# Performance work log

Measured on AMD Instinct MI355X. Metric: run time of the kernel, lower is better.

Reference implementation:

```python
import jax, jax.numpy as jnp
import numpy as np

N_NODES = 50000

# DGL ChebConv with k=2 and the standard lambda_max=2 approximation:
#   L_hat = L - I = -D^{-1/2} A D^{-1/2}
#   X0 = X ; X1 = L_hat @ X ; out = concat([X0, X1], -1) @ W + b
# Norm uses in-degrees (DGL behavior).

def setup_inputs() -> dict:
    key = jax.random.key(0)
    ks = jax.random.split(key, 8)
    E = 800000
    src = jax.random.randint(ks[0], (E,), 0, N_NODES, dtype=jnp.int32)
    dst = jax.random.randint(ks[1], (E,), 0, N_NODES, dtype=jnp.int32)
    def w(k, shape):
        fan_in = shape[0]
        return jax.random.normal(k, shape, jnp.float32) * (1.0 / np.sqrt(fan_in))
    return {
        "x": jax.random.normal(ks[2], (N_NODES, 128), jnp.float32),
        "src": src, "dst": dst,
        "W1": w(ks[3], (256, 256)), "b1": jnp.zeros((256,), jnp.float32),
        "W2": w(ks[4], (512, 256)), "b2": jnp.zeros((256,), jnp.float32),
        "W3": w(ks[5], (512, 128)), "b3": jnp.zeros((128,), jnp.float32),
    }

def _cheb_layer(h, src, dst, dinv, W, b):
    # X1 = -D^{-1/2} A D^{-1/2} h  (lambda_max = 2)
    hn = h * dinv[:, None]
    agg = jax.ops.segment_sum(hn[src], dst, num_segments=N_NODES)
    x1 = -(agg * dinv[:, None])
    return jnp.concatenate([h, x1], axis=-1) @ W + b

def reference(x, src, dst, W1, b1, W2, b2, W3, b3):
    deg = jax.ops.segment_sum(jnp.ones_like(dst, dtype=x.dtype), dst,
                              num_segments=N_NODES)
    dinv = jnp.where(deg > 0, jax.lax.rsqrt(jnp.maximum(deg, 1.0)), 0.0)
    h = jnp.tanh(_cheb_layer(x, src, dst, dinv, W1, b1))
    for _ in range(3):  # hid_layer = 3
        h = jnp.tanh(_cheb_layer(h, src, dst, dinv, W2, b2))
    return _cheb_layer(h, src, dst, dinv, W3, b3)
```

## Files before the change

### kernel.cpp

```cpp
#include <hip/hip_runtime.h>
#include <cmath>

#define NN 50000
#define CAP 64

typedef short v8s __attribute__((ext_vector_type(8)));
typedef float v4f __attribute__((ext_vector_type(4)));

__device__ __forceinline__ float b2f(unsigned short u) {
    return __uint_as_float(((unsigned int)u) << 16);
}
__device__ __forceinline__ unsigned short f2b(float f) {
    unsigned int x = __float_as_uint(f);
    x += 0x7fffu + ((x >> 16) & 1u);
    return (unsigned short)(x >> 16);
}

__device__ __forceinline__ void gld16(const void* g, void* l) {
    __builtin_amdgcn_global_load_lds(
        (const __attribute__((address_space(1))) unsigned int*)g,
        (__attribute__((address_space(3))) unsigned int*)l, 16, 0, 0);
}

__global__ void sniff_kernel(const unsigned short* __restrict__ x, int* __restrict__ mode) {
    if (threadIdx.x == 0 && blockIdx.x == 0) {
        int c = 0;
        for (int i = 0; i < 128; ++i) {
            unsigned int e = (x[i] >> 7) & 0xFFu;
            if (e >= 100u && e <= 140u) ++c;
        }
        *mode = (c >= 112) ? 0 : 1;
    }
}

__global__ void fill_kernel(const int* __restrict__ src, const int* __restrict__ dst,
                            int* __restrict__ cnt, unsigned short* __restrict__ ell, int E) {
    int e = blockIdx.x * blockDim.x + threadIdx.x;
    if (e < E) {
        int d = dst[e];
        int pos = atomicAdd(&cnt[d], 1);
        if (pos < CAP) ell[d * CAP + pos] = (unsigned short)src[e];
    }
}

__global__ void dinv_kernel(const int* __restrict__ cnt, float* __restrict__ dinv, int n) {
    int i = blockIdx.x * blockDim.x + threadIdx.x;
    if (i < n) {
        int d = cnt[i];
        dinv[i] = (d > 0) ? rsqrtf((float)d) : 0.0f;
    }
}

__global__ void prep_kernel(const void* __restrict__ x,
                            const void* __restrict__ W1, const void* __restrict__ W2,
                            const void* __restrict__ W3, const void* __restrict__ b1,
                            const void* __restrict__ b2, const void* __restrict__ b3,
                            unsigned short* __restrict__ buf,
                            unsigned short* __restrict__ WT1, unsigned short* __restrict__ WT2,
                            unsigned short* __restrict__ WT3, unsigned short* __restrict__ bb1,
                            unsigned short* __restrict__ bb2, unsigned short* __restrict__ bb3,
                            const int* __restrict__ modep) {
    int mode = *modep;
    int b = blockIdx.x, t = threadIdx.x;
    if (b < 3125) {
        int idx = b * 256 + t;
        int n = idx >> 4, c = idx & 15;
        if (mode == 0) {
            ((uint4*)buf)[n * 64 + c] = ((const uint4*)x)[idx];
        } else {
            const float* xf = (const float*)x + (size_t)idx * 8;
            unsigned short o[8];
#pragma unroll
            for (int i = 0; i < 8; ++i) o[i] = f2b(xf[i]);
            ((uint4*)buf)[n * 64 + c] = *(const uint4*)o;
        }
    } else if (b < 3381) {
        int idx = (b - 3125) * 256 + t;
        int n = idx >> 8, k = idx & 255;
        WT1[idx] = mode ? f2b(((const float*)W1)[k * 256 + n])
                        : ((const unsigned short*)W1)[k * 256 + n];
    } else if (b < 3893) {
        int idx = (b - 3381) * 256 + t;
        int n = idx >> 9, k = idx & 511;
        WT2[idx] = mode ? f2b(((const float*)W2)[k * 256 + n])
                        : ((const unsigned short*)W2)[k * 256 + n];
    } else if (b < 4149) {
        int idx = (b - 3893) * 256 + t;
        int n = idx >> 9, k = idx & 511;
        WT3[idx] = mode ? f2b(((const float*)W3)[k * 128 + n])
                        : ((const unsigned short*)W3)[k * 128 + n];
    } else {
        if (t < 256) {
            bb1[t] = mode ? f2b(((const float*)b1)[t]) : ((const unsigned short*)b1)[t];
            bb2[t] = mode ? f2b(((const float*)b2)[t]) : ((const unsigned short*)b2)[t];
        }
        if (t < 128)
            bb3[t] = mode ? f2b(((const float*)b3)[t]) : ((const unsigned short*)b3)[t];
    }
}

template <int FPL>
__global__ void spmm_kernel(const unsigned short* __restrict__ h, int ldh,
                            const int* __restrict__ cnt, const unsigned short* __restrict__ ell,
                            const float* __restrict__ dinv,
                            unsigned short* __restrict__ out, int ldo) {
    int node = blockIdx.x * 4 + (threadIdx.x >> 6);
    int lane = threadIdx.x & 63;
    int c = cnt[node]; c = (c < CAP) ? c : CAP;
    int sl = (int)ell[node * CAP + lane];
    float dl = dinv[sl];
    float acc[FPL];
#pragma unroll
    for (int i = 0; i < FPL; ++i) acc[i] = 0.f;
    const int col = lane * FPL;

    int g = 0;
    for (; g + 8 <= c; g += 8) {
        int s[8]; float d[8];
#pragma unroll
        for (int i = 0; i < 8; ++i) { s[i] = __shfl(sl, g + i); d[i] = __shfl(dl, g + i); }
        if (FPL == 4) {
            ushort4 v[8];
#pragma unroll
            for (int i = 0; i < 8; ++i)
                v[i] = *(const ushort4*)(h + (size_t)s[i] * ldh + col);
#pragma unroll
            for (int i = 0; i < 8; ++i) {
                acc[0] += d[i] * b2f(v[i].x); acc[1] += d[i] * b2f(v[i].y);
                acc[2] += d[i] * b2f(v[i].z); acc[3] += d[i] * b2f(v[i].w);
            }
        } else {
            ushort2 v[8];
#pragma unroll
            for (int i = 0; i < 8; ++i)
                v[i] = *(const ushort2*)(h + (size_t)s[i] * ldh + col);
#pragma unroll
            for (int i = 0; i < 8; ++i) {
                acc[0] += d[i] * b2f(v[i].x); acc[1] += d[i] * b2f(v[i].y);
            }
        }
    }
    for (; g < c; ++g) {
        int sg = __shfl(sl, g);
        float dg = __shfl(dl, g);
        const unsigned short* hp = h + (size_t)sg * ldh + col;
        if (FPL == 4) {
            ushort4 v = *(const ushort4*)hp;
            acc[0] += dg * b2f(v.x); acc[1] += dg * b2f(v.y);
            acc[2] += dg * b2f(v.z); acc[3] += dg * b2f(v.w);
        } else {
            ushort2 v = *(const ushort2*)hp;
            acc[0] += dg * b2f(v.x); acc[1] += dg * b2f(v.y);
        }
    }

    float dn = -dinv[node];
    unsigned short* op = out + (size_t)node * ldo + col;
    if (FPL == 4) {
        ushort4 o;
        o.x = f2b(acc[0] * dn); o.y = f2b(acc[1] * dn);
        o.z = f2b(acc[2] * dn); o.w = f2b(acc[3] * dn);
        *(ushort4*)op = o;
    } else {
        ushort2 o;
        o.x = f2b(acc[0] * dn); o.y = f2b(acc[1] * dn);
        *(ushort2*)op = o;
    }
}

template <int K32, int NQ>
__global__ void gemm_lds_kernel(const unsigned short* __restrict__ A, int lda,
                                const unsigned short* __restrict__ WT,
                                const unsigned short* __restrict__ bias,
                                void* __restrict__ out, int ldo,
                                int M, int dotanh, int is_final, const int* __restrict__ modep) {
    constexpr int K    = K32 * 32;
    constexpr int NB   = NQ * 64;
    constexpr int NTHR = 2 * NQ * 64;
    constexpr int ACH  = 128 * 4;
    constexpr int BCH  = NB * 4;
    constexpr int ROUNDS = (ACH + BCH) / NTHR;
    __shared__ unsigned short lds[(128 + NB) * 32];

    const int tid = threadIdx.x;
    const int wave = tid >> 6, lane = tid & 63, quad = lane >> 4, l16 = lane & 15;
    const int mh = wave / NQ, nq = wave % NQ;
    const int m0 = blockIdx.x * 128;

    v4f acc[4][4];
#pragma unroll
    for (int mi = 0; mi < 4; ++mi)
#pragma unroll
        for (int ni = 0; ni < 4; ++ni) acc[mi][ni] = (v4f){0.f, 0.f, 0.f, 0.f};

    const unsigned short* gp[ROUNDS];
#pragma unroll
    for (int r = 0; r < ROUNDS; ++r) {
        int c = tid + r * NTHR;
        if (c < ACH) {
            int row = m0 + (c >> 2);
            if (row >= M) row = M - 1;
            gp[r] = A + (size_t)row * lda + (c & 3) * 8;
        } else {
            int cb = c - ACH;
            gp[r] = WT + (size_t)(cb >> 2) * K + (cb & 3) * 8;
        }
    }

    const unsigned short* aT = lds;
    const unsigned short* bT = lds + 128 * 32;

    for (int k0 = 0; k0 < K; k0 += 32) {
#pragma unroll
        for (int r = 0; r < ROUNDS; ++r) {
            int c = tid + r * NTHR;
            gld16(gp[r] + k0, (void*)&lds[c * 8]);
        }
        __syncthreads();

        v8s a_frag[4], b_frag[4];
#pragma unroll
        for (int mi = 0; mi < 4; ++mi)
            a_frag[mi] = *(const v8s*)&aT[(mh * 64 + mi * 16 + l16) * 32 + quad * 8];
#pragma unroll
        for (int ni = 0; ni < 4; ++ni)
            b_frag[ni] = *(const v8s*)&bT[(nq * 64 + ni * 16 + l16) * 32 + quad * 8];
#pragma unroll
        for (int mi = 0; mi < 4; ++mi)
#pragma unroll
            for (int ni = 0; ni < 4; ++ni)
                acc[mi][ni] = __builtin_amdgcn_mfma_f32_16x16x32_bf16(a_frag[mi], b_frag[ni],
                                                                      acc[mi][ni], 0, 0, 0);
        __syncthreads();
    }

    int fin = is_final ? *modep : 0;
#pragma unroll
    for (int ni = 0; ni < 4; ++ni) {
        int colc = nq * 64 + ni * 16 + l16;
        float bv = b2f(bias[colc]);
#pragma unroll
        for (int mi = 0; mi < 4; ++mi) {
#pragma unroll
            for (int r = 0; r < 4; ++r) {
                int row = m0 + mh * 64 + mi * 16 + quad * 4 + r;
                if (row < M) {
                    float v = acc[mi][ni][r] + bv;
                    if (dotanh) v = tanhf(v);
                    if (fin) ((float*)out)[(size_t)row * ldo + colc] = v;
                    else     ((unsigned short*)out)[(size_t)row * ldo + colc] = f2b(v);
                }
            }
        }
    }
}

static inline size_t al256(size_t x) { return (x + 255) & ~(size_t)255; }

extern "C" void kernel_launch(void* const* d_in, const int* in_sizes, int n_in,
                              void* d_out, int out_size, void* d_ws, size_t ws_size,
                              hipStream_t stream) {
    const void* x  = d_in[0];
    const int* src = (const int*)d_in[1];
    const int* dst = (const int*)d_in[2];
    const void* W1 = d_in[3]; const void* b1 = d_in[4];
    const void* W2 = d_in[5]; const void* b2 = d_in[6];
    const void* W3 = d_in[7]; const void* b3 = d_in[8];
    const int E = in_sizes[1];

    char* p = (char*)d_ws;
    int* mode     = (int*)p;            p += 256;
    int* cnt      = (int*)p;            p += al256((size_t)NN * 4);
    float* dinv   = (float*)p;          p += al256((size_t)NN * 4);
    unsigned short* ell = (unsigned short*)p; p += al256((size_t)NN * CAP * 2);
    unsigned short* WT1 = (unsigned short*)p; p += al256((size_t)256 * 256 * 2);
    unsigned short* WT2 = (unsigned short*)p; p += al256((size_t)256 * 512 * 2);
    unsigned short* WT3 = (unsigned short*)p; p += al256((size_t)128 * 512 * 2);
    unsigned short* bb1 = (unsigned short*)p; p += al256((size_t)256 * 2);
    unsigned short* bb2 = (unsigned short*)p; p += al256((size_t)256 * 2);
    unsigned short* bb3 = (unsigned short*)p; p += al256((size_t)128 * 2);
    unsigned short* buf = (unsigned short*)p; p += al256((size_t)NN * 512 * 2);

    hipMemsetAsync(cnt, 0, (size_t)NN * 4, stream);
    sniff_kernel<<<1, 64, 0, stream>>>((const unsigned short*)x, mode);
    prep_kernel<<<4150, 256, 0, stream>>>(x, W1, W2, W3, b1, b2, b3,
                                          buf, WT1, WT2, WT3, bb1, bb2, bb3, mode);
    int eb = (E + 255) / 256;
    fill_kernel<<<eb, 256, 0, stream>>>(src, dst, cnt, ell, E);
    dinv_kernel<<<(NN + 255) / 256, 256, 0, stream>>>(cnt, dinv, NN);

    const int SPMM_GRID = NN / 4;
    const int GB = (NN + 127) / 128;

    spmm_kernel<2><<<SPMM_GRID, 256, 0, stream>>>(buf, 512, cnt, ell, dinv, buf + 128, 512);
    gemm_lds_kernel<8, 4><<<GB, 512, 0, stream>>>(buf, 512, WT1, bb1, buf, 512, NN, 1, 0, mode);
    spmm_kernel<4><<<SPMM_GRID, 256, 0, stream>>>(buf, 512, cnt, ell, dinv, buf + 256, 512);
    gemm_lds_kernel<16, 4><<<GB, 512, 0, stream>>>(buf, 512, WT2, bb2, buf, 512, NN, 1, 0, mode);
    spmm_kernel<4><<<SPMM_GRID, 256, 0, stream>>>(buf, 512, cnt, ell, dinv, buf + 256, 512);
    gemm_lds_kernel<16, 4><<<GB, 512, 0, stream>>>(buf, 512, WT2, bb2, buf, 512, NN, 1, 0, mode);
    spmm_kernel<4><<<SPMM_GRID, 256, 0, stream>>>(buf, 512, cnt, ell, dinv, buf + 256, 512);
    gemm_lds_kernel<16, 4><<<GB, 512, 0, stream>>>(buf, 512, WT2, bb2, buf, 512, NN, 1, 0, mode);
    spmm_kernel<4><<<SPMM_GRID, 256, 0, stream>>>(buf, 512, cnt, ell, dinv, buf + 256, 512);
    gemm_lds_kernel<16, 2><<<GB, 256, 0, stream>>>(buf, 512, WT3, bb3, d_out, 128, NN, 0, 1, mode);
}
```

Measured before the change: 555.1 us.

## Store activations in 32-column panels and gather per panel in SpMM

Activations move from a row-major 512-wide buffer into separate 32-column panels, each NN x 32. The SpMM kernel now runs one block per panel and node group, so each gather touches a compact 64-byte row and the working set of a panel can stay in cache. Each wave handles 4 nodes and splits edges across 8 lane groups, then combines the partial sums with xor shuffles. The GEMM loads A from the panels by striding PSTR per k-step and writes its output back in panel layout, while the final layer keeps its row-major output. In exchange there are many more SpMM blocks, extra reductions, and the GEMM A loads become strided across panels.

```diff
diff --git a/kernel.cpp b/kernel.cpp
--- a/kernel.cpp
+++ b/kernel.cpp
@@ -3,6 +3,8 @@
 
 #define NN 50000
 #define CAP 64
+
+constexpr int PSTR = NN * 32;
 
 typedef short v8s __attribute__((ext_vector_type(8)));
 typedef float v4f __attribute__((ext_vector_type(4)));
@@ -65,14 +67,15 @@
     if (b < 3125) {
         int idx = b * 256 + t;
         int n = idx >> 4, c = idx & 15;
+        uint4* dp = (uint4*)(buf + (size_t)(8 + (c >> 2)) * PSTR + (size_t)n * 32 + (c & 3) * 8);
         if (mode == 0) {
-            ((uint4*)buf)[n * 64 + c] = ((const uint4*)x)[idx];
+            *dp = ((const uint4*)x)[idx];
         } else {
             const float* xf = (const float*)x + (size_t)idx * 8;
             unsigned short o[8];
 #pragma unroll
             for (int i = 0; i < 8; ++i) o[i] = f2b(xf[i]);
-            ((uint4*)buf)[n * 64 + c] = *(const uint4*)o;
+            *dp = *(const uint4*)o;
         }
     } else if (b < 3381) {
         int idx = (b - 3125) * 256 + t;
@@ -99,77 +102,56 @@
     }
 }
 
-template <int FPL>
-__global__ void spmm_kernel(const unsigned short* __restrict__ h, int ldh,
-                            const int* __restrict__ cnt, const unsigned short* __restrict__ ell,
+template <int NP>
+__global__ void spmm_kernel(const unsigned short* __restrict__ hp,
+                            const int* __restrict__ cnt,
+                            const unsigned short* __restrict__ ell,
                             const float* __restrict__ dinv,
-                            unsigned short* __restrict__ out, int ldo) {
-    int node = blockIdx.x * 4 + (threadIdx.x >> 6);
-    int lane = threadIdx.x & 63;
-    int c = cnt[node]; c = (c < CAP) ? c : CAP;
-    int sl = (int)ell[node * CAP + lane];
-    float dl = dinv[sl];
-    float acc[FPL];
-#pragma unroll
-    for (int i = 0; i < FPL; ++i) acc[i] = 0.f;
-    const int col = lane * FPL;
-
-    int g = 0;
-    for (; g + 8 <= c; g += 8) {
-        int s[8]; float d[8];
-#pragma unroll
-        for (int i = 0; i < 8; ++i) { s[i] = __shfl(sl, g + i); d[i] = __shfl(dl, g + i); }
-        if (FPL == 4) {
-            ushort4 v[8];
-#pragma unroll
-            for (int i = 0; i < 8; ++i)
-                v[i] = *(const ushort4*)(h + (size_t)s[i] * ldh + col);
-#pragma unroll
-            for (int i = 0; i < 8; ++i) {
-                acc[0] += d[i] * b2f(v[i].x); acc[1] += d[i] * b2f(v[i].y);
-                acc[2] += d[i] * b2f(v[i].z); acc[3] += d[i] * b2f(v[i].w);
-            }
-        } else {
-            ushort2 v[8];
-#pragma unroll
-            for (int i = 0; i < 8; ++i)
-                v[i] = *(const ushort2*)(h + (size_t)s[i] * ldh + col);
-#pragma unroll
-            for (int i = 0; i < 8; ++i) {
-                acc[0] += d[i] * b2f(v[i].x); acc[1] += d[i] * b2f(v[i].y);
-            }
-        }
-    }
-    for (; g < c; ++g) {
-        int sg = __shfl(sl, g);
-        float dg = __shfl(dl, g);
-        const unsigned short* hp = h + (size_t)sg * ldh + col;
-        if (FPL == 4) {
-            ushort4 v = *(const ushort4*)hp;
-            acc[0] += dg * b2f(v.x); acc[1] += dg * b2f(v.y);
-            acc[2] += dg * b2f(v.z); acc[3] += dg * b2f(v.w);
-        } else {
-            ushort2 v = *(const ushort2*)hp;
-            acc[0] += dg * b2f(v.x); acc[1] += dg * b2f(v.y);
-        }
-    }
-
-    float dn = -dinv[node];
-    unsigned short* op = out + (size_t)node * ldo + col;
-    if (FPL == 4) {
-        ushort4 o;
-        o.x = f2b(acc[0] * dn); o.y = f2b(acc[1] * dn);
-        o.z = f2b(acc[2] * dn); o.w = f2b(acc[3] * dn);
-        *(ushort4*)op = o;
-    } else {
-        ushort2 o;
-        o.x = f2b(acc[0] * dn); o.y = f2b(acc[1] * dn);
-        *(ushort2*)op = o;
+                            unsigned short* __restrict__ outp) {
+    const int panel = blockIdx.x & (NP - 1);
+    const int grp   = blockIdx.x / NP;
+    const int lane  = threadIdx.x & 63;
+    const int wave  = threadIdx.x >> 6;
+    const int gid   = lane >> 3;
+    const int fid   = lane & 7;
+    const unsigned short* hb = hp + (size_t)panel * PSTR;
+    unsigned short* ob = outp + (size_t)panel * PSTR;
+    const int node0 = (grp * 4 + wave) * 4;
+
+#pragma unroll
+    for (int ni = 0; ni < 4; ++ni) {
+        int node = node0 + ni;
+        if (node >= NN) return;
+        int c = cnt[node]; c = (c < CAP) ? c : CAP;
+        int sl = (int)ell[node * CAP + lane];
+        float dl = dinv[sl];
+        float a0 = 0.f, a1 = 0.f, a2 = 0.f, a3 = 0.f;
+        for (int e = 0; e < c; e += 8) {
+            int idx = e + gid;
+            int s   = __shfl(sl, idx & 63);
+            float d = __shfl(dl, idx & 63);
+            if (idx >= c) { s = 0; d = 0.f; }
+            const ushort4 v = *(const ushort4*)(hb + ((size_t)s << 5) + (fid << 2));
+            a0 += d * b2f(v.x); a1 += d * b2f(v.y);
+            a2 += d * b2f(v.z); a3 += d * b2f(v.w);
+        }
+#pragma unroll
+        for (int m = 8; m < 64; m <<= 1) {
+            a0 += __shfl_xor(a0, m); a1 += __shfl_xor(a1, m);
+            a2 += __shfl_xor(a2, m); a3 += __shfl_xor(a3, m);
+        }
+        if (lane < 8) {
+            float dn = -dinv[node];
+            ushort4 o;
+            o.x = f2b(a0 * dn); o.y = f2b(a1 * dn);
+            o.z = f2b(a2 * dn); o.w = f2b(a3 * dn);
+            *(ushort4*)(ob + ((size_t)node << 5) + (lane << 2)) = o;
+        }
     }
 }
 
 template <int K32, int NQ>
-__global__ void gemm_lds_kernel(const unsigned short* __restrict__ A, int lda,
+__global__ void gemm_lds_kernel(const unsigned short* __restrict__ A,
                                 const unsigned short* __restrict__ WT,
                                 const unsigned short* __restrict__ bias,
                                 void* __restrict__ out, int ldo,
@@ -200,7 +182,7 @@
         if (c < ACH) {
             int row = m0 + (c >> 2);
             if (row >= M) row = M - 1;
-            gp[r] = A + (size_t)row * lda + (c & 3) * 8;
+            gp[r] = A + (size_t)row * 32 + (c & 3) * 8;
         } else {
             int cb = c - ACH;
             gp[r] = WT + (size_t)(cb >> 2) * K + (cb & 3) * 8;
@@ -210,12 +192,14 @@
     const unsigned short* aT = lds;
     const unsigned short* bT = lds + 128 * 32;
 
+    int koffA = 0, koffB = 0;
     for (int k0 = 0; k0 < K; k0 += 32) {
 #pragma unroll
         for (int r = 0; r < ROUNDS; ++r) {
             int c = tid + r * NTHR;
-            gld16(gp[r] + k0, (void*)&lds[c * 8]);
-        }
+            gld16(gp[r] + ((r * NTHR) < ACH ? koffA : koffB), (void*)&lds[c * 8]);
+        }
+        koffA += PSTR; koffB += 32;
         __syncthreads();
 
         v8s a_frag[4], b_frag[4];
@@ -234,11 +218,12 @@
         __syncthreads();
     }
 
-    int fin = is_final ? *modep : 0;
+    int fin = is_final ? (*modep ? 2 : 1) : 0;
 #pragma unroll
     for (int ni = 0; ni < 4; ++ni) {
         int colc = nq * 64 + ni * 16 + l16;
         float bv = b2f(bias[colc]);
+        size_t pbase = (size_t)(colc >> 5) * PSTR + (colc & 31);
 #pragma unroll
         for (int mi = 0; mi < 4; ++mi) {
 #pragma unroll
@@ -247,8 +232,9 @@
                 if (row < M) {
                     float v = acc[mi][ni][r] + bv;
                     if (dotanh) v = tanhf(v);
-                    if (fin) ((float*)out)[(size_t)row * ldo + colc] = v;
-                    else     ((unsigned short*)out)[(size_t)row * ldo + colc] = f2b(v);
+                    if (fin == 2)      ((float*)out)[(size_t)row * ldo + colc] = v;
+                    else if (fin == 1) ((unsigned short*)out)[(size_t)row * ldo + colc] = f2b(v);
+                    else               ((unsigned short*)out)[pbase + ((size_t)row << 5)] = f2b(v);
                 }
             }
         }
@@ -279,7 +265,7 @@
     unsigned short* bb1 = (unsigned short*)p; p += al256((size_t)256 * 2);
     unsigned short* bb2 = (unsigned short*)p; p += al256((size_t)256 * 2);
     unsigned short* bb3 = (unsigned short*)p; p += al256((size_t)128 * 2);
-    unsigned short* buf = (unsigned short*)p; p += al256((size_t)NN * 512 * 2);
+    unsigned short* buf = (unsigned short*)p; p += al256((size_t)16 * PSTR * 2);
 
     hipMemsetAsync(cnt, 0, (size_t)NN * 4, stream);
     sniff_kernel<<<1, 64, 0, stream>>>((const unsigned short*)x, mode);
@@ -289,17 +275,20 @@
     fill_kernel<<<eb, 256, 0, stream>>>(src, dst, cnt, ell, E);
     dinv_kernel<<<(NN + 255) / 256, 256, 0, stream>>>(cnt, dinv, NN);
 
-    const int SPMM_GRID = NN / 4;
-    const int GB = (NN + 127) / 128;
-
-    spmm_kernel<2><<<SPMM_GRID, 256, 0, stream>>>(buf, 512, cnt, ell, dinv, buf + 128, 512);
-    gemm_lds_kernel<8, 4><<<GB, 512, 0, stream>>>(buf, 512, WT1, bb1, buf, 512, NN, 1, 0, mode);
-    spmm_kernel<4><<<SPMM_GRID, 256, 0, stream>>>(buf, 512, cnt, ell, dinv, buf + 256, 512);
-    gemm_lds_kernel<16, 4><<<GB, 512, 0, stream>>>(buf, 512, WT2, bb2, buf, 512, NN, 1, 0, mode);
-    spmm_kernel<4><<<SPMM_GRID, 256, 0, stream>>>(buf, 512, cnt, ell, dinv, buf + 256, 512);
-    gemm_lds_kernel<16, 4><<<GB, 512, 0, stream>>>(buf, 512, WT2, bb2, buf, 512, NN, 1, 0, mode);
-    spmm_kernel<4><<<SPMM_GRID, 256, 0, stream>>>(buf, 512, cnt, ell, dinv, buf + 256, 512);
-    gemm_lds_kernel<16, 4><<<GB, 512, 0, stream>>>(buf, 512, WT2, bb2, buf, 512, NN, 1, 0, mode);
-    spmm_kernel<4><<<SPMM_GRID, 256, 0, stream>>>(buf, 512, cnt, ell, dinv, buf + 256, 512);
-    gemm_lds_kernel<16, 2><<<GB, 256, 0, stream>>>(buf, 512, WT3, bb3, d_out, 128, NN, 0, 1, mode);
-}
+    const int SG8 = 8 * 3125;
+    const int SG4 = 4 * 3125;
+    const int GB  = (NN + 127) / 128;
+
+    spmm_kernel<4><<<SG4, 256, 0, stream>>>(buf + (size_t)8 * PSTR, cnt, ell, dinv,
+                                            buf + (size_t)12 * PSTR);
+    gemm_lds_kernel<8, 4><<<GB, 512, 0, stream>>>(buf + (size_t)8 * PSTR, WT1, bb1,
+                                                  buf, 0, NN, 1, 0, mode);
+    spmm_kernel<8><<<SG8, 256, 0, stream>>>(buf, cnt, ell, dinv, buf + (size_t)8 * PSTR);
+    gemm_lds_kernel<16, 4><<<GB, 512, 0, stream>>>(buf, WT2, bb2, buf, 0, NN, 1, 0, mode);
+    spmm_kernel<8><<<SG8, 256, 0, stream>>>(buf, cnt, ell, dinv, buf + (size_t)8 * PSTR);
+    gemm_lds_kernel<16, 4><<<GB, 512, 0, stream>>>(buf, WT2, bb2, buf, 0, NN, 1, 0, mode);
+    spmm_kernel<8><<<SG8, 256, 0, stream>>>(buf, cnt, ell, dinv, buf + (size_t)8 * PSTR);
+    gemm_lds_kernel<16, 4><<<GB, 512, 0, stream>>>(buf, WT2, bb2, buf, 0, NN, 1, 0, mode);
+    spmm_kernel<8><<<SG8, 256, 0, stream>>>(buf, cnt, ell, dinv, buf + (size_t)8 * PSTR);
+    gemm_lds_kernel<16, 2><<<GB, 256, 0, stream>>>(buf, WT3, bb3, d_out, 128, NN, 0, 1, mode);
+}
```

Result: slower. 824.0 us (+48.4%).
